# Optimization experiments

Measured on AMD Instinct MI355X. Metric: run time of the kernel, lower is better.

Reference implementation:

```python
import jax, jax.numpy as jnp
import numpy as np

B, T, C = 2, 2048, 1024
N_HEAD = 16
HEAD_DIM = C // N_HEAD


def setup_inputs() -> dict:
    key = jax.random.key(0)
    ks = jax.random.split(key, 5)
    s = 0.02
    return {
        "x": jax.random.normal(ks[0], (B, T, C), dtype=jnp.float32),
        "W_kqv": jax.random.normal(ks[1], (C, 3 * C), dtype=jnp.float32) * s,
        "b_kqv": jax.random.normal(ks[2], (3 * C,), dtype=jnp.float32) * s,
        "W_proj": jax.random.normal(ks[3], (C, C), dtype=jnp.float32) * s,
        "b_proj": jax.random.normal(ks[4], (C,), dtype=jnp.float32) * s,
    }


def reference(x, W_kqv, b_kqv, W_proj, b_proj):
    Bx, Tx, Cx = x.shape
    qkv = x @ W_kqv + b_kqv                      # [B, T, 3C]
    q, k, v = jnp.split(qkv, 3, axis=-1)
    # [B, H, T, D]
    q = q.reshape(Bx, Tx, N_HEAD, HEAD_DIM).transpose(0, 2, 1, 3)
    k = k.reshape(Bx, Tx, N_HEAD, HEAD_DIM).transpose(0, 2, 1, 3)
    v = v.reshape(Bx, Tx, N_HEAD, HEAD_DIM).transpose(0, 2, 1, 3)
    scale = 1.0 / jnp.sqrt(jnp.asarray(HEAD_DIM, dtype=x.dtype))
    att = jnp.einsum("bhqd,bhkd->bhqk", q, k) * scale  # [B, H, T, T]
    causal = jnp.tril(jnp.ones((Tx, Tx), dtype=bool))   # [T, T]
    att = jnp.where(causal[None, None], att, jnp.float32(-jnp.inf))
    att = jax.nn.softmax(att, axis=-1)
    y = jnp.einsum("bhqk,bhkd->bhqd", att, v)            # [B, H, T, D]
    y = y.transpose(0, 2, 1, 3).reshape(Bx, Tx, Cx)
    out = y @ W_proj + b_proj
    return out, k, v
```

## Files before the change

kernel.cpp:

```cpp
#include <hip/hip_runtime.h>


#define DEVI __device__ __forceinline__

typedef unsigned short ushort_t;
typedef unsigned long long u64_t;
typedef __attribute__((ext_vector_type(4))) unsigned short us4;
typedef __attribute__((ext_vector_type(8))) unsigned short ushort8;
typedef __attribute__((ext_vector_type(4))) float f32x4;
typedef __attribute__((ext_vector_type(8))) __bf16 bf16x8;

DEVI unsigned short f2bf(float f) {
  union { float f; unsigned int u; } c; c.f = f;
  unsigned int u = c.u;
  unsigned int r = (u + 0x7FFFu + ((u >> 16) & 1u)) >> 16;
  return (unsigned short)r;
}

DEVI float exp2v(float x) {
  float r;
  asm("v_exp_f32 %0, %1\n\ts_nop 0" : "=v"(r) : "v"(x));
  return r;
}

DEVI unsigned int cvtpk(float lo, float hi) {
  unsigned int r;
  asm("v_cvt_pk_bf16_f32 %0, %1, %2" : "=v"(r) : "v"(lo), "v"(hi));
  return r;
}

DEVI f32x4 mfma16(ushort8 a, ushort8 b, f32x4 c) {
  return __builtin_amdgcn_mfma_f32_16x16x32_bf16(
      __builtin_bit_cast(bf16x8, a), __builtin_bit_cast(bf16x8, b), c, 0, 0, 0);
}

typedef const __attribute__((address_space(1))) void* gptr_t;
typedef __attribute__((address_space(3))) void* lptr_t;
#define GLOAD_LDS16(g, l) \
  __builtin_amdgcn_global_load_lds((gptr_t)(g), (lptr_t)(l), 16, 0, 0)

DEVI void bar() {
  asm volatile("" ::: "memory");
  __builtin_amdgcn_s_barrier();
  asm volatile("" ::: "memory");
}
#define VMCNT(n) asm volatile("s_waitcnt vmcnt(" #n ")" ::: "memory")


__global__ void prep_kernel(const float* __restrict__ x,
                            const float* __restrict__ Wk,
                            const float* __restrict__ Wp,
                            ushort_t* __restrict__ Xb,
                            ushort_t* __restrict__ Wkt,
                            ushort_t* __restrict__ Wpt) {
  __shared__ float tile[32][33];
  const int id = blockIdx.x, tid = threadIdx.x;
  if (id < 2048) {
    const int i = id * 256 + tid;
    const f32x4* p = (const f32x4*)x;
    f32x4 a = p[2 * i], b = p[2 * i + 1];
    ushort8 o;
    o[0] = f2bf(a[0]); o[1] = f2bf(a[1]); o[2] = f2bf(a[2]); o[3] = f2bf(a[3]);
    o[4] = f2bf(b[0]); o[5] = f2bf(b[1]); o[6] = f2bf(b[2]); o[7] = f2bf(b[3]);
    ((ushort8*)Xb)[i] = o;
    return;
  }
  const float* in;
  ushort_t* outp;
  int R = 1024, Cin, bx, by;
  if (id < 5120) {
    const int jid = id - 2048;
    bx = jid % 96; by = jid / 96; in = Wk; outp = Wkt; Cin = 3072;
  } else {
    const int jid = id - 5120;
    bx = jid % 32; by = jid / 32; in = Wp; outp = Wpt; Cin = 1024;
  }
  const int c0 = bx * 32, r0 = by * 32;
  const int tx = tid & 31, ty = tid >> 5;
#pragma unroll
  for (int it = 0; it < 4; ++it)
    tile[ty + it * 8][tx] = in[(size_t)(r0 + ty + it * 8) * Cin + c0 + tx];
  __syncthreads();
#pragma unroll
  for (int it = 0; it < 4; ++it)
    outp[(size_t)(c0 + ty + it * 8) * R + r0 + tx] = f2bf(tile[tx][ty + it * 8]);
}


__global__ __launch_bounds__(256) void gemm_bt_kernel(
    const ushort_t* __restrict__ A, const ushort_t* __restrict__ Bt,
    const float* __restrict__ bias, float* __restrict__ outF,
    float* __restrict__ outK, float* __restrict__ outV,
    ushort_t* __restrict__ Qb, ushort_t* __restrict__ Kb, ushort_t* __restrict__ Vb,
    int M, int N, int K, int mode) {
  __shared__ __align__(16) ushort_t As[128 * 64];
  __shared__ __align__(16) ushort_t Bs[128 * 64];
  const int tid = threadIdx.x;
  const int w = tid >> 6, lane = tid & 63;
  const int wr = w >> 1, wc = w & 1;
  const int nbx = gridDim.x;
  const int nwg = nbx * gridDim.y;
  const int orig = blockIdx.x + nbx * blockIdx.y;
  const int tile = (orig & 7) * (nwg >> 3) + (orig >> 3);
  const int bx = tile % nbx, by = tile / nbx;
  const int m0 = by * 128, n0 = bx * 128;
  const int l15 = lane & 15, lhi = lane >> 4;
  const int rowA = lane >> 3;
  const int sgc = (((lane & 7) ^ ((lane >> 3) & 7)) << 3);

  f32x4 acc[4][4] = {};

  const int nk = K >> 6;
  for (int kt = 0; kt < nk; ++kt) {
    const size_t k0 = (size_t)kt << 6;
    if (kt) bar();
#pragma unroll
    for (int it = 0; it < 4; ++it) {
      const int rbase = (w * 4 + it) * 8;
      GLOAD_LDS16(A + (size_t)(m0 + rbase + rowA) * K + k0 + sgc, &As[rbase * 64]);
      GLOAD_LDS16(Bt + (size_t)(n0 + rbase + rowA) * K + k0 + sgc, &Bs[rbase * 64]);
    }
    VMCNT(0);
    bar();
#pragma unroll
    for (int kk = 0; kk < 2; ++kk) {
      const int gof = (((kk * 4 + lhi) ^ (l15 & 7)) << 3);
      ushort8 a[4], b[4];
#pragma unroll
      for (int i = 0; i < 4; ++i)
        a[i] = *(const ushort8*)&As[(wr * 64 + i * 16 + l15) * 64 + gof];
#pragma unroll
      for (int j = 0; j < 4; ++j)
        b[j] = *(const ushort8*)&Bs[(wc * 64 + j * 16 + l15) * 64 + gof];
#pragma unroll
      for (int i = 0; i < 4; ++i)
#pragma unroll
        for (int j = 0; j < 4; ++j) acc[i][j] = mfma16(a[i], b[j], acc[i][j]);
    }
  }

  const float QSCALE = 0.18033688011112042f;
#pragma unroll
  for (int i = 0; i < 4; ++i) {
#pragma unroll
    for (int j = 0; j < 4; ++j) {
      const int nn = n0 + wc * 64 + j * 16 + l15;
      const float bv = bias[nn];
#pragma unroll
      for (int r = 0; r < 4; ++r) {
        const int mm = m0 + wr * 64 + i * 16 + lhi * 4 + r;
        const float v = acc[i][j][r] + bv;
        if (mode == 0) {
          outF[(size_t)mm * N + nn] = v;
        } else {
          const int bb = mm >> 11, t = mm & 2047;
          const int c = nn & 1023, h = c >> 6, d = c & 63;
          const size_t idx = ((size_t)(bb * 16 + h) * 2048 + t) * 64 + d;
          const int sec = nn >> 10;
          if (sec == 0) {
            Qb[idx] = f2bf(v * QSCALE);
          } else if (sec == 1) {
            outK[idx] = v; Kb[idx] = f2bf(v);
          } else {
            outV[idx] = v; Vb[idx] = f2bf(v);
          }
        }
      }
    }
  }
}


__global__ __launch_bounds__(256) void gemm_bt64_kernel(
    const ushort_t* __restrict__ A, const ushort_t* __restrict__ Bt,
    const float* __restrict__ bias, float* __restrict__ outF,
    int M, int N, int K) {
  __shared__ __align__(16) ushort_t As[64 * 64];
  __shared__ __align__(16) ushort_t Bs[128 * 64];
  const int tid = threadIdx.x;
  const int w = tid >> 6, lane = tid & 63;
  const int wr = w >> 1, wc = w & 1;
  const int nbx = gridDim.x;
  const int nwg = nbx * gridDim.y;
  const int orig = blockIdx.x + nbx * blockIdx.y;
  const int tile = (orig & 7) * (nwg >> 3) + (orig >> 3);
  const int bx = tile % nbx, by = tile / nbx;
  const int m0 = by * 64, n0 = bx * 128;
  const int l15 = lane & 15, lhi = lane >> 4;
  const int rowA = lane >> 3;
  const int sgc = (((lane & 7) ^ ((lane >> 3) & 7)) << 3);

  f32x4 acc[2][4] = {};

  const int nk = K >> 6;
  for (int kt = 0; kt < nk; ++kt) {
    const size_t k0 = (size_t)kt << 6;
    if (kt) bar();
#pragma unroll
    for (int it = 0; it < 2; ++it) {
      const int rbase = (w * 2 + it) * 8;
      GLOAD_LDS16(A + (size_t)(m0 + rbase + rowA) * K + k0 + sgc, &As[rbase * 64]);
    }
#pragma unroll
    for (int it = 0; it < 4; ++it) {
      const int rbase = (w * 4 + it) * 8;
      GLOAD_LDS16(Bt + (size_t)(n0 + rbase + rowA) * K + k0 + sgc, &Bs[rbase * 64]);
    }
    VMCNT(0);
    bar();
#pragma unroll
    for (int kk = 0; kk < 2; ++kk) {
      const int gof = (((kk * 4 + lhi) ^ (l15 & 7)) << 3);
      ushort8 a[2], b[4];
#pragma unroll
      for (int i = 0; i < 2; ++i)
        a[i] = *(const ushort8*)&As[(wr * 32 + i * 16 + l15) * 64 + gof];
#pragma unroll
      for (int j = 0; j < 4; ++j)
        b[j] = *(const ushort8*)&Bs[(wc * 64 + j * 16 + l15) * 64 + gof];
#pragma unroll
      for (int i = 0; i < 2; ++i)
#pragma unroll
        for (int j = 0; j < 4; ++j) acc[i][j] = mfma16(a[i], b[j], acc[i][j]);
    }
  }

#pragma unroll
  for (int i = 0; i < 2; ++i) {
#pragma unroll
    for (int j = 0; j < 4; ++j) {
      const int nn = n0 + wc * 64 + j * 16 + l15;
      const float bv = bias[nn];
#pragma unroll
      for (int r = 0; r < 4; ++r) {
        const int mm = m0 + wr * 32 + i * 16 + lhi * 4 + r;
        outF[(size_t)mm * N + nn] = acc[i][j][r] + bv;
      }
    }
  }
}


__global__ __launch_bounds__(256) void attn_kernel(
    const ushort_t* __restrict__ Qb, const ushort_t* __restrict__ Kb,
    const ushort_t* __restrict__ Vb, ushort_t* __restrict__ Yb) {
  __shared__ __align__(16) ushort_t Ks[2][64 * 64];
  __shared__ __align__(16) ushort_t Vt[2][64 * 72];
  __shared__ __align__(16) ushort_t Pl[4 * 16 * 72];
  const int id = blockIdx.x;
  const int xcd = id & 7, win = id >> 3;
  const int qt = 31 - (win >> 2);
  const int bh = xcd + 8 * (win & 3);
  const int b = bh >> 4, h = bh & 15;
  const int tid = threadIdx.x, w = tid >> 6, lane = tid & 63;
  const int l15 = lane & 15, lhi = lane >> 4;
  const int swzP = 2 * (l15 & 3);
  const size_t base = (size_t)bh * 2048 * 64;
  const float NEG_INF = -__builtin_inff();
  ushort_t* myP = &Pl[w * 16 * 72];

  const int vd0 = (tid & 15) * 4;
  const int vt0b = (tid >> 4) * 2;

  const int nkt = qt + 1;

  ushort8 qf[2];
  {
    const size_t qrow = base + (size_t)(qt * 64 + w * 16 + l15) * 64;
    qf[0] = *(const ushort8*)&Qb[qrow + lhi * 8];
    qf[1] = *(const ushort8*)&Qb[qrow + 32 + lhi * 8];
  }
  float m_s = NEG_INF, l_s = 0.f;
  f32x4 o[4] = {};

  {
#pragma unroll
    for (int it = 0; it < 2; ++it) {
      const int chunk = tid + it * 256;
      const int row = chunk >> 3, g = chunk & 7;
      const int sg = g ^ (row & 7);
      GLOAD_LDS16(Kb + base + (size_t)row * 64 + sg * 8, &Ks[0][chunk * 8]);
    }
#pragma unroll
    for (int it = 0; it < 2; ++it) {
      const int t0 = vt0b + it * 32;
      const ushort_t* vp = Vb + base + (size_t)t0 * 64 + vd0;
      u64_t a = *(const u64_t*)vp;
      u64_t c = *(const u64_t*)(vp + 64);
      us4 av = __builtin_bit_cast(us4, a);
      us4 cv = __builtin_bit_cast(us4, c);
#pragma unroll
      for (int i = 0; i < 4; ++i) {
        const int d = vd0 + i;
        const int scg = (t0 >> 3) ^ ((d >> 3) & 7);
        unsigned int wv = (unsigned int)av[i] | ((unsigned int)cv[i] << 16);
        *(unsigned int*)&Vt[0][d * 72 + scg * 8 + (t0 & 7)] = wv;
      }
    }
  }
  __syncthreads();

  for (int kt = 0; kt < nkt; ++kt) {
    const int cur = kt & 1, nxt = cur ^ 1;
    const bool pf = (kt + 1 < nkt);
    u64_t va[2], vc[2];
    if (pf) {
      const size_t tb = base + (size_t)(kt + 1) * 64 * 64;
#pragma unroll
      for (int it = 0; it < 2; ++it) {
        const int chunk = tid + it * 256;
        const int row = chunk >> 3, g = chunk & 7;
        const int sg = g ^ (row & 7);
        GLOAD_LDS16(Kb + tb + (size_t)row * 64 + sg * 8, &Ks[nxt][chunk * 8]);
      }
#pragma unroll
      for (int it = 0; it < 2; ++it) {
        const int t0 = vt0b + it * 32;
        const ushort_t* vp = Vb + tb + (size_t)t0 * 64 + vd0;
        va[it] = *(const u64_t*)vp;
        vc[it] = *(const u64_t*)(vp + 64);
      }
    }

    f32x4 s[4] = {};
    __builtin_amdgcn_s_setprio(1);
#pragma unroll
    for (int kk = 0; kk < 2; ++kk) {
#pragma unroll
      for (int j = 0; j < 4; ++j) {
        const int g = (kk * 4 + lhi) ^ (l15 & 7);
        ushort8 kb = *(const ushort8*)&Ks[cur][(j * 16 + l15) * 64 + g * 8];
        s[j] = mfma16(kb, qf[kk], s[j]);
      }
    }
    __builtin_amdgcn_s_setprio(0);
    const int qloc = w * 16 + l15;
    if (kt == qt) {
#pragma unroll
      for (int j = 0; j < 4; ++j)
#pragma unroll
        for (int r = 0; r < 4; ++r)
          if ((j * 16 + lhi * 4 + r) > qloc) s[j][r] = NEG_INF;
    }

    float pmax = s[0][0];
#pragma unroll
    for (int j = 0; j < 4; ++j)
#pragma unroll
      for (int r = 0; r < 4; ++r) pmax = fmaxf(pmax, s[j][r]);
    pmax = fmaxf(pmax, __shfl_xor(pmax, 16));
    pmax = fmaxf(pmax, __shfl_xor(pmax, 32));
    if (__any(pmax - m_s > 8.0f)) {
      const float mnew = fmaxf(m_s, pmax);
      const float al = exp2v(m_s - mnew);
      m_s = mnew;
      l_s *= al;
#pragma unroll
      for (int df = 0; df < 4; ++df)
#pragma unroll
        for (int r = 0; r < 4; ++r) o[df][r] *= al;
    }
    float rsum = 0.f;
#pragma unroll
    for (int j = 0; j < 4; ++j)
#pragma unroll
      for (int r = 0; r < 4; ++r) {
        const float pe = exp2v(s[j][r] - m_s);
        s[j][r] = pe;
        rsum += pe;
      }
    rsum += __shfl_xor(rsum, 16);
    rsum += __shfl_xor(rsum, 32);
    l_s += rsum;

#pragma unroll
    for (int j = 0; j < 4; ++j) {
      const unsigned int w0 = cvtpk(s[j][0], s[j][1]);
      const unsigned int w1 = cvtpk(s[j][2], s[j][3]);
      const u64_t dw = (u64_t)w0 | ((u64_t)w1 << 32);
      const int cg = j * 2 + (lhi >> 1);
      *(u64_t*)&myP[l15 * 72 + ((cg ^ swzP) << 3) + ((lhi & 1) << 2)] = dw;
    }

    __builtin_amdgcn_s_setprio(1);
#pragma unroll
    for (int kk = 0; kk < 2; ++kk) {
      ushort8 pa = *(const ushort8*)&myP[l15 * 72 + (((kk * 4 + lhi) ^ swzP) << 3)];
#pragma unroll
      for (int df = 0; df < 4; ++df) {
        const int r = df * 16 + l15;
        const int g = (kk * 4 + lhi) ^ ((r >> 3) & 7);
        ushort8 vb = *(const ushort8*)&Vt[cur][r * 72 + g * 8];
        o[df] = mfma16(vb, pa, o[df]);
      }
    }
    __builtin_amdgcn_s_setprio(0);

    if (pf) {
#pragma unroll
      for (int it = 0; it < 2; ++it) {
        const int t0 = vt0b + it * 32;
        us4 av = __builtin_bit_cast(us4, va[it]);
        us4 cv = __builtin_bit_cast(us4, vc[it]);
#pragma unroll
        for (int i = 0; i < 4; ++i) {
          const int d = vd0 + i;
          const int scg = (t0 >> 3) ^ ((d >> 3) & 7);
          unsigned int wv = (unsigned int)av[i] | ((unsigned int)cv[i] << 16);
          *(unsigned int*)&Vt[nxt][d * 72 + scg * 8 + (t0 & 7)] = wv;
        }
      }
    }
    __syncthreads();
  }

  const float inv = 1.0f / l_s;
  const size_t yrow = (size_t)(b * 2048 + qt * 64 + w * 16 + l15) * 1024 + h * 64;
#pragma unroll
  for (int df = 0; df < 4; ++df) {
    us4 ov;
#pragma unroll
    for (int r = 0; r < 4; ++r) ov[r] = f2bf(o[df][r] * inv);
    *(us4*)&Yb[yrow + df * 16 + lhi * 4] = ov;
  }
}


extern "C" void kernel_launch(void* const* d_in, const int* in_sizes, int n_in,
                              void* d_out, int out_size, void* d_ws, size_t ws_size,
                              hipStream_t stream) {
  const float* x      = (const float*)d_in[0];
  const float* W_kqv  = (const float*)d_in[1];
  const float* b_kqv  = (const float*)d_in[2];
  const float* W_proj = (const float*)d_in[3];
  const float* b_proj = (const float*)d_in[4];
  float* out  = (float*)d_out;
  float* outK = out + 4194304;
  float* outV = out + 8388608;

  char* ws = (char*)d_ws;
  ushort_t* Xb  = (ushort_t*)(ws);
  ushort_t* Wkt = (ushort_t*)(ws + ((size_t)8 << 20));
  ushort_t* Wpt = (ushort_t*)(ws + ((size_t)14 << 20));
  ushort_t* Qb  = (ushort_t*)(ws + ((size_t)16 << 20));
  ushort_t* Kb  = (ushort_t*)(ws + ((size_t)24 << 20));
  ushort_t* Vb  = (ushort_t*)(ws + ((size_t)32 << 20));
  ushort_t* Yb  = Xb;

  prep_kernel<<<6144, 256, 0, stream>>>(x, W_kqv, W_proj, Xb, Wkt, Wpt);
  gemm_bt_kernel<<<dim3(24, 32), 256, 0, stream>>>(
      Xb, Wkt, b_kqv, nullptr, outK, outV, Qb, Kb, Vb, 4096, 3072, 1024, 1);
  attn_kernel<<<1024, 256, 0, stream>>>(Qb, Kb, Vb, Yb);
  gemm_bt64_kernel<<<dim3(8, 64), 256, 0, stream>>>(
      Yb, Wpt, b_proj, out, 4096, 1024, 1024);
}
```

Baseline: 110.3 us.

## Use 128-row query tiles with 8-wave attention blocks sharing K/V tiles

```diff
diff --git a/kernel.cpp b/kernel.cpp
--- a/kernel.cpp
+++ b/kernel.cpp
@@ -241,15 +241,15 @@
 }
 
 
-__global__ __launch_bounds__(256) void attn_kernel(
+__global__ __launch_bounds__(512) void attn_kernel(
     const ushort_t* __restrict__ Qb, const ushort_t* __restrict__ Kb,
     const ushort_t* __restrict__ Vb, ushort_t* __restrict__ Yb) {
   __shared__ __align__(16) ushort_t Ks[2][64 * 64];
   __shared__ __align__(16) ushort_t Vt[2][64 * 72];
-  __shared__ __align__(16) ushort_t Pl[4 * 16 * 72];
+  __shared__ __align__(16) ushort_t Pl[8 * 16 * 72];
   const int id = blockIdx.x;
   const int xcd = id & 7, win = id >> 3;
-  const int qt = 31 - (win >> 2);
+  const int qt = 15 - (win >> 2);
   const int bh = xcd + 8 * (win & 3);
   const int b = bh >> 4, h = bh & 15;
   const int tid = threadIdx.x, w = tid >> 6, lane = tid & 63;
@@ -259,43 +259,36 @@
   const float NEG_INF = -__builtin_inff();
   ushort_t* myP = &Pl[w * 16 * 72];
 
+  const int krow = tid >> 3, kg = tid & 7;
+  const int ksg = kg ^ (krow & 7);
   const int vd0 = (tid & 15) * 4;
-  const int vt0b = (tid >> 4) * 2;
-
-  const int nkt = qt + 1;
+  const int vt0 = (tid >> 4) * 2;
+
+  const int nkt = 2 * qt + 2;
+  const int qrow = w * 16 + l15;
 
   ushort8 qf[2];
   {
-    const size_t qrow = base + (size_t)(qt * 64 + w * 16 + l15) * 64;
-    qf[0] = *(const ushort8*)&Qb[qrow + lhi * 8];
-    qf[1] = *(const ushort8*)&Qb[qrow + 32 + lhi * 8];
+    const size_t qrg = base + (size_t)(qt * 128 + qrow) * 64;
+    qf[0] = *(const ushort8*)&Qb[qrg + lhi * 8];
+    qf[1] = *(const ushort8*)&Qb[qrg + 32 + lhi * 8];
   }
   float m_s = NEG_INF, l_s = 0.f;
   f32x4 o[4] = {};
 
   {
-#pragma unroll
-    for (int it = 0; it < 2; ++it) {
-      const int chunk = tid + it * 256;
-      const int row = chunk >> 3, g = chunk & 7;
-      const int sg = g ^ (row & 7);
-      GLOAD_LDS16(Kb + base + (size_t)row * 64 + sg * 8, &Ks[0][chunk * 8]);
-    }
-#pragma unroll
-    for (int it = 0; it < 2; ++it) {
-      const int t0 = vt0b + it * 32;
-      const ushort_t* vp = Vb + base + (size_t)t0 * 64 + vd0;
-      u64_t a = *(const u64_t*)vp;
-      u64_t c = *(const u64_t*)(vp + 64);
-      us4 av = __builtin_bit_cast(us4, a);
-      us4 cv = __builtin_bit_cast(us4, c);
-#pragma unroll
-      for (int i = 0; i < 4; ++i) {
-        const int d = vd0 + i;
-        const int scg = (t0 >> 3) ^ ((d >> 3) & 7);
-        unsigned int wv = (unsigned int)av[i] | ((unsigned int)cv[i] << 16);
-        *(unsigned int*)&Vt[0][d * 72 + scg * 8 + (t0 & 7)] = wv;
-      }
+    GLOAD_LDS16(Kb + base + (size_t)krow * 64 + ksg * 8, &Ks[0][tid * 8]);
+    const ushort_t* vp = Vb + base + (size_t)vt0 * 64 + vd0;
+    u64_t a = *(const u64_t*)vp;
+    u64_t c = *(const u64_t*)(vp + 64);
+    us4 av = __builtin_bit_cast(us4, a);
+    us4 cv = __builtin_bit_cast(us4, c);
+#pragma unroll
+    for (int i = 0; i < 4; ++i) {
+      const int d = vd0 + i;
+      const int scg = (vt0 >> 3) ^ ((d >> 3) & 7);
+      unsigned int wv = (unsigned int)av[i] | ((unsigned int)cv[i] << 16);
+      *(unsigned int*)&Vt[0][d * 72 + scg * 8 + (vt0 & 7)] = wv;
     }
   }
   __syncthreads();
@@ -303,27 +296,16 @@
   for (int kt = 0; kt < nkt; ++kt) {
     const int cur = kt & 1, nxt = cur ^ 1;
     const bool pf = (kt + 1 < nkt);
-    u64_t va[2], vc[2];
+    u64_t va = 0, vc = 0;
     if (pf) {
       const size_t tb = base + (size_t)(kt + 1) * 64 * 64;
-#pragma unroll
-      for (int it = 0; it < 2; ++it) {
-        const int chunk = tid + it * 256;
-        const int row = chunk >> 3, g = chunk & 7;
-        const int sg = g ^ (row & 7);
-        GLOAD_LDS16(Kb + tb + (size_t)row * 64 + sg * 8, &Ks[nxt][chunk * 8]);
-      }
-#pragma unroll
-      for (int it = 0; it < 2; ++it) {
-        const int t0 = vt0b + it * 32;
-        const ushort_t* vp = Vb + tb + (size_t)t0 * 64 + vd0;
-        va[it] = *(const u64_t*)vp;
-        vc[it] = *(const u64_t*)(vp + 64);
-      }
+      GLOAD_LDS16(Kb + tb + (size_t)krow * 64 + ksg * 8, &Ks[nxt][tid * 8]);
+      const ushort_t* vp = Vb + tb + (size_t)vt0 * 64 + vd0;
+      va = *(const u64_t*)vp;
+      vc = *(const u64_t*)(vp + 64);
     }
 
     f32x4 s[4] = {};
-    __builtin_amdgcn_s_setprio(1);
 #pragma unroll
     for (int kk = 0; kk < 2; ++kk) {
 #pragma unroll
@@ -333,14 +315,13 @@
         s[j] = mfma16(kb, qf[kk], s[j]);
       }
     }
-    __builtin_amdgcn_s_setprio(0);
-    const int qloc = w * 16 + l15;
-    if (kt == qt) {
+    if (64 * kt + 63 > 128 * qt + w * 16) {
+      const int delta = 128 * qt + qrow - 64 * kt;
 #pragma unroll
       for (int j = 0; j < 4; ++j)
 #pragma unroll
         for (int r = 0; r < 4; ++r)
-          if ((j * 16 + lhi * 4 + r) > qloc) s[j][r] = NEG_INF;
+          if ((j * 16 + lhi * 4 + r) > delta) s[j][r] = NEG_INF;
     }
 
     float pmax = s[0][0];
@@ -382,7 +363,6 @@
       *(u64_t*)&myP[l15 * 72 + ((cg ^ swzP) << 3) + ((lhi & 1) << 2)] = dw;
     }
 
-    __builtin_amdgcn_s_setprio(1);
 #pragma unroll
     for (int kk = 0; kk < 2; ++kk) {
       ushort8 pa = *(const ushort8*)&myP[l15 * 72 + (((kk * 4 + lhi) ^ swzP) << 3)];
@@ -394,28 +374,23 @@
         o[df] = mfma16(vb, pa, o[df]);
       }
     }
-    __builtin_amdgcn_s_setprio(0);
 
     if (pf) {
-#pragma unroll
-      for (int it = 0; it < 2; ++it) {
-        const int t0 = vt0b + it * 32;
-        us4 av = __builtin_bit_cast(us4, va[it]);
-        us4 cv = __builtin_bit_cast(us4, vc[it]);
-#pragma unroll
-        for (int i = 0; i < 4; ++i) {
-          const int d = vd0 + i;
-          const int scg = (t0 >> 3) ^ ((d >> 3) & 7);
-          unsigned int wv = (unsigned int)av[i] | ((unsigned int)cv[i] << 16);
-          *(unsigned int*)&Vt[nxt][d * 72 + scg * 8 + (t0 & 7)] = wv;
-        }
+      us4 av = __builtin_bit_cast(us4, va);
+      us4 cv = __builtin_bit_cast(us4, vc);
+#pragma unroll
+      for (int i = 0; i < 4; ++i) {
+        const int d = vd0 + i;
+        const int scg = (vt0 >> 3) ^ ((d >> 3) & 7);
+        unsigned int wv = (unsigned int)av[i] | ((unsigned int)cv[i] << 16);
+        *(unsigned int*)&Vt[nxt][d * 72 + scg * 8 + (vt0 & 7)] = wv;
       }
     }
     __syncthreads();
   }
 
   const float inv = 1.0f / l_s;
-  const size_t yrow = (size_t)(b * 2048 + qt * 64 + w * 16 + l15) * 1024 + h * 64;
+  const size_t yrow = (size_t)(b * 2048 + qt * 128 + qrow) * 1024 + h * 64;
 #pragma unroll
   for (int df = 0; df < 4; ++df) {
     us4 ov;
@@ -450,7 +425,7 @@
   prep_kernel<<<6144, 256, 0, stream>>>(x, W_kqv, W_proj, Xb, Wkt, Wpt);
   gemm_bt_kernel<<<dim3(24, 32), 256, 0, stream>>>(
       Xb, Wkt, b_kqv, nullptr, outK, outV, Qb, Kb, Vb, 4096, 3072, 1024, 1);
-  attn_kernel<<<1024, 256, 0, stream>>>(Qb, Kb, Vb, Yb);
+  attn_kernel<<<512, 512, 0, stream>>>(Qb, Kb, Vb, Yb);
   gemm_bt64_kernel<<<dim3(8, 64), 256, 0, stream>>>(
       Yb, Wpt, b_proj, out, 4096, 1024, 1024);
 }
```

New measurement: 108.8 us. No clear change (-1.4%).
